# Kernel tuning notes

Measured on AMD Instinct MI355X. Metric: run time of the kernel, lower is better.

The kernel has to match this reference:

```python
import jax, jax.numpy as jnp
import numpy as np

HID = 1024
DEPTH = 2

def _rhn_layer(x, Win, bin_, Wh, bh, Wt, bt):
    # x: [B, T, in]; returns outputs [B, T, H]
    B = x.shape[0]
    h0 = jnp.zeros((B, HID), dtype=x.dtype)
    xt = jnp.swapaxes(x, 0, 1)  # [T, B, in]

    def step(h_prev, x_t):
        h = x_t @ Win + bin_
        for i in range(DEPTH):
            t_gate = jax.nn.sigmoid(h @ Wt[i] + bt[i])
            h_layer = jnp.tanh(h @ Wh[i] + bh[i])
            h = t_gate * h_layer + (1.0 - t_gate) * h
        h_new = h + h_prev
        return h_new, h_new

    _, outs = jax.lax.scan(step, h0, xt)  # [T, B, H]
    return jnp.swapaxes(outs, 0, 1)


def setup_inputs() -> dict:
    key = jax.random.key(0)
    ks = jax.random.split(key, 16)
    B, T, IN, H, OUT = 64, 256, 128, HID, 128
    s = lambda fan_in: 1.0 / np.sqrt(fan_in)
    d = {}
    d["x"] = jax.random.normal(ks[0], (B, T, IN), dtype=jnp.float32)
    # layer 0 (input_size=IN)
    d["l0_Win"] = jax.random.uniform(ks[1], (IN, H), minval=-s(IN), maxval=s(IN))
    d["l0_bin"] = jax.random.uniform(ks[2], (H,), minval=-s(IN), maxval=s(IN))
    d["l0_Wh"] = jax.random.uniform(ks[3], (DEPTH, H, H), minval=-s(H), maxval=s(H))
    d["l0_bh"] = jax.random.uniform(ks[4], (DEPTH, H), minval=-s(H), maxval=s(H))
    d["l0_Wt"] = jax.random.uniform(ks[5], (DEPTH, H, H), minval=-s(H), maxval=s(H))
    d["l0_bt"] = jax.random.uniform(ks[6], (DEPTH, H), minval=-s(H), maxval=s(H))
    # layer 1 (input_size=H)
    d["l1_Win"] = jax.random.uniform(ks[7], (H, H), minval=-s(H), maxval=s(H))
    d["l1_bin"] = jax.random.uniform(ks[8], (H,), minval=-s(H), maxval=s(H))
    d["l1_Wh"] = jax.random.uniform(ks[9], (DEPTH, H, H), minval=-s(H), maxval=s(H))
    d["l1_bh"] = jax.random.uniform(ks[10], (DEPTH, H), minval=-s(H), maxval=s(H))
    d["l1_Wt"] = jax.random.uniform(ks[11], (DEPTH, H, H), minval=-s(H), maxval=s(H))
    d["l1_bt"] = jax.random.uniform(ks[12], (DEPTH, H), minval=-s(H), maxval=s(H))
    # final fc
    d["fc_W"] = jax.random.uniform(ks[13], (H, OUT), minval=-s(H), maxval=s(H))
    d["fc_b"] = jax.random.uniform(ks[14], (OUT,), minval=-s(H), maxval=s(H))
    return d


def reference(x, l0_Win, l0_bin, l0_Wh, l0_bh, l0_Wt, l0_bt,
              l1_Win, l1_bin, l1_Wh, l1_bh, l1_Wt, l1_bt, fc_W, fc_b):
    out = _rhn_layer(x, l0_Win, l0_bin, l0_Wh, l0_bh, l0_Wt, l0_bt)
    out = _rhn_layer(out, l1_Win, l1_bin, l1_Wh, l1_bh, l1_Wt, l1_bt)
    # forecast_horizon = 1 -> last time step only
    out = out[:, -1:, :] @ fc_W + fc_b  # [B, 1, OUT]
    return out
```

## Files before the change

kernel.cpp:

```cpp
#include <hip/hip_runtime.h>

typedef unsigned short u16;
typedef unsigned int u32;
typedef __bf16 bf16x8 __attribute__((ext_vector_type(8)));
typedef float floatx4 __attribute__((ext_vector_type(4)));

#define HID 1024
#define BATCH 64
#define SEQ 256
#define INDIM 128
#define OUTDIM 128
#define MROWS (BATCH*SEQ)
#define CUMP 140

__device__ __forceinline__ float b2f(u16 u) {
    union { u32 u; float f; } v; v.u = ((u32)u) << 16; return v.f;
}
__device__ __forceinline__ u16 f2b(float f) {
    union { float f; u32 u; } v; v.f = f;
    u32 x = v.u;
    x += 0x7fffu + ((x >> 16) & 1u);
    return (u16)(x >> 16);
}
__device__ __forceinline__ float sigm(float x) { return 1.f / (1.f + __expf(-x)); }
__device__ __forceinline__ float tanh_f(float x) { return 2.f / (1.f + __expf(-2.f * x)) - 1.f; }

__device__ __forceinline__ void gld16(const u16* g, u16* l) {
    __builtin_amdgcn_global_load_lds(
        (const __attribute__((address_space(1))) void*)g,
        (__attribute__((address_space(3))) void*)l, 16, 0, 0);
}

__device__ __forceinline__ void bar_sync() {
    asm volatile("" ::: "memory");
    __builtin_amdgcn_s_barrier();
    asm volatile("" ::: "memory");
}
template <int N>
__device__ __forceinline__ void vm_bar() {
    asm volatile("s_waitcnt vmcnt(%0)" :: "n"(N) : "memory");
    __builtin_amdgcn_s_barrier();
    asm volatile("" ::: "memory");
}

__device__ __forceinline__ int is_fp32(const u16* probe, int tid) {
    const int lane = tid & 63;
    const int e = (probe[lane * 7] >> 7) & 0xff;
    return __ballot(e >= 127) != 0ULL;
}

struct CvtList { const void* s[8]; u16* d[8]; int n[8]; };

__global__ void convert8(CvtList C, const u16* __restrict__ probe) {
    const int fp32 = is_fp32(probe, threadIdx.x);
    const int z = blockIdx.y;
    const int n = C.n[z];
    const int stride = gridDim.x * 256;
    for (int i = blockIdx.x * 256 + threadIdx.x; i < n; i += stride) {
        u16 o;
        if (fp32) o = f2b(((const float*)C.s[z])[i]);
        else      o = ((const u16*)C.s[z])[i];
        C.d[z][i] = o;
    }
}

struct TListO {
    const void* s[10];
    u16*        d[10];
    int         R[10];
    int         Cc[10];
    long        off[10];
};

__global__ void transpose10(TListO L, const u16* __restrict__ probe) {
    const int tx = threadIdx.x, ty = threadIdx.y;
    const int fp32 = is_fp32(probe, ty * 32 + tx);
    const int z = blockIdx.z;
    const void* src = L.s[z];
    u16*        dst = L.d[z];
    const int R  = L.R[z];
    const int Cc = L.Cc[z];
    const long zo = L.off[z];
    const int tr = blockIdx.y * 32, tc = blockIdx.x * 32;
    if (tr >= R || tc >= Cc) return;
    __align__(16) __shared__ u16 t[32][33];
#pragma unroll
    for (int i = 0; i < 4; ++i) {
        const int r = ty + i * 8;
        const long e = zo + (long)(tr + r) * Cc + tc + tx;
        u16 v;
        if (fp32) v = f2b(((const float*)src)[e]);
        else      v = ((const u16*)src)[e];
        t[r][tx] = v;
    }
    __syncthreads();
#pragma unroll
    for (int i = 0; i < 4; ++i) {
        const int r = ty + i * 8;
        dst[(size_t)(tc + r) * R + tr + tx] = t[tx][r];
    }
}

__device__ __forceinline__ void tile_swizzle(int& m0, int& n0) {
    const int lin = blockIdx.y * gridDim.x + blockIdx.x;
    const int xcd = lin & 7;
    const int loc = lin >> 3;
    m0 = (xcd * 16 + (loc & 15)) * 128;
    n0 = (loc >> 4) * 128;
}

__device__ __forceinline__ void tile_swizzle8(int& m0, int& n0) {
    const int lin = blockIdx.x;
    const int xcd = lin & 7;
    const int loc = lin >> 3;
    m0 = (xcd * 8 + (loc & 7)) * 256;
    n0 = (loc >> 3) * 128;
}

__global__ __launch_bounds__(256, 2) void gemm128(
    const u16* __restrict__ A, const u16* __restrict__ BT,
    const u16* __restrict__ bias, u16* __restrict__ C,
    int M, int N, int K)
{
    __align__(16) __shared__ u16 As[128 * 64];
    __align__(16) __shared__ u16 Bs[128 * 64];

    const int tid  = threadIdx.x;
    const int lane = tid & 63;
    const int wid  = tid >> 6;
    const int wr   = wid >> 1;
    const int wc   = wid & 1;

    int m0, n0;
    tile_swizzle(m0, n0);

    floatx4 acc[4][4] = {};

    const int srow = lane >> 3;
    const int scol = 8 * ((lane & 7) ^ (lane >> 3));
    const int cb   = wid * 4;
    const u16* Ag[4]; const u16* Bg[4];
    u16 *Al[4], *Bl[4];
#pragma unroll
    for (int j = 0; j < 4; ++j) {
        const int c = cb + j;
        const int r = c * 8 + srow;
        Ag[j] = A  + (size_t)(m0 + r) * K + scol;
        Bg[j] = BT + (size_t)(n0 + r) * K + scol;
        Al[j] = As + c * 512;
        Bl[j] = Bs + c * 512;
    }

    const int quad = lane >> 4;
    const int l16  = lane & 15;
    const int swz  = l16 & 7;

    const int nk = K >> 6;
    for (int kt = 0; kt < nk; ++kt) {
        __syncthreads();
#pragma unroll
        for (int j = 0; j < 4; ++j) {
            gld16(Ag[j], Al[j]);  gld16(Bg[j], Bl[j]);
            Ag[j] += 64; Bg[j] += 64;
        }
        __syncthreads();

#pragma unroll
        for (int kk = 0; kk < 2; ++kk) {
            const int slot = ((kk * 4 + quad) ^ swz) * 8;
            bf16x8 af[4], bfr[4];
#pragma unroll
            for (int i = 0; i < 4; ++i) {
                af[i]  = *(const bf16x8*)(As + (wr * 64 + i * 16 + l16) * 64 + slot);
                bfr[i] = *(const bf16x8*)(Bs + (wc * 64 + i * 16 + l16) * 64 + slot);
            }
#pragma unroll
            for (int i = 0; i < 4; ++i)
#pragma unroll
                for (int j = 0; j < 4; ++j)
                    acc[i][j] = __builtin_amdgcn_mfma_f32_16x16x32_bf16(af[i], bfr[j], acc[i][j], 0, 0, 0);
        }
    }

#pragma unroll
    for (int i = 0; i < 4; ++i) {
        const int rowb = m0 + wr * 64 + i * 16 + quad * 4;
#pragma unroll
        for (int j = 0; j < 4; ++j) {
            const int col = n0 + wc * 64 + j * 16 + l16;
            const float bv = b2f(bias[col]);
#pragma unroll
            for (int r = 0; r < 4; ++r)
                C[(size_t)(rowb + r) * N + col] = f2b(acc[i][j][r] + bv);
        }
    }
}

__global__ __launch_bounds__(256, 2) void gemm_wp(
    const u16* __restrict__ At, const u16* __restrict__ Ah,
    const u16* __restrict__ BT, u16* __restrict__ Ct, u16* __restrict__ Ch)
{
    const u16* A = blockIdx.y ? Ah : At;
    u16*       C = blockIdx.y ? Ch : Ct;
    const int m0 = blockIdx.x * 128;
    const int K = HID, N = 128;

    __align__(16) __shared__ u16 As[128 * 64];
    __align__(16) __shared__ u16 Bs[128 * 64];

    const int tid  = threadIdx.x;
    const int lane = tid & 63;
    const int wid  = tid >> 6;
    const int wr   = wid >> 1;
    const int wc   = wid & 1;

    floatx4 acc[4][4] = {};

    const int srow = lane >> 3;
    const int scol = 8 * ((lane & 7) ^ (lane >> 3));
    const int cb   = wid * 4;
    const u16* Ag[4]; const u16* Bg[4];
    u16 *Al[4], *Bl[4];
#pragma unroll
    for (int j = 0; j < 4; ++j) {
        const int c = cb + j;
        const int r = c * 8 + srow;
        Ag[j] = A  + (size_t)(m0 + r) * K + scol;
        Bg[j] = BT + (size_t)r * K + scol;
        Al[j] = As + c * 512;
        Bl[j] = Bs + c * 512;
    }

    const int quad = lane >> 4;
    const int l16  = lane & 15;
    const int swz  = l16 & 7;

    for (int kt = 0; kt < (K >> 6); ++kt) {
        __syncthreads();
#pragma unroll
        for (int j = 0; j < 4; ++j) {
            gld16(Ag[j], Al[j]);  gld16(Bg[j], Bl[j]);
            Ag[j] += 64; Bg[j] += 64;
        }
        __syncthreads();

#pragma unroll
        for (int kk = 0; kk < 2; ++kk) {
            const int slot = ((kk * 4 + quad) ^ swz) * 8;
            bf16x8 af[4], bfr[4];
#pragma unroll
            for (int i = 0; i < 4; ++i) {
                af[i]  = *(const bf16x8*)(As + (wr * 64 + i * 16 + l16) * 64 + slot);
                bfr[i] = *(const bf16x8*)(Bs + (wc * 64 + i * 16 + l16) * 64 + slot);
            }
#pragma unroll
            for (int i = 0; i < 4; ++i)
#pragma unroll
                for (int j = 0; j < 4; ++j)
                    acc[i][j] = __builtin_amdgcn_mfma_f32_16x16x32_bf16(af[i], bfr[j], acc[i][j], 0, 0, 0);
        }
    }

#pragma unroll
    for (int i = 0; i < 4; ++i) {
        const int rowb = m0 + wr * 64 + i * 16 + quad * 4;
#pragma unroll
        for (int j = 0; j < 4; ++j) {
            const int col = wc * 64 + j * 16 + l16;
#pragma unroll
            for (int r = 0; r < 4; ++r)
                C[(size_t)(rowb + r) * N + col] = f2b(acc[i][j][r]);
        }
    }
}

__global__ void bias_fold(const u16* __restrict__ tWt, const u16* __restrict__ tWh,
                          const u16* __restrict__ binv, const u16* __restrict__ bt0,
                          const u16* __restrict__ bh0,
                          u16* __restrict__ obt, u16* __restrict__ obh)
{
    const u16* tW = blockIdx.y ? tWh : tWt;
    const u16* bo = blockIdx.y ? bh0 : bt0;
    u16*       ob = blockIdx.y ? obh : obt;
    const int j = blockIdx.x * 128 + threadIdx.x;
    const u16* row = tW + (size_t)j * HID;
    float acc = 0.f;
    for (int k = 0; k < HID; k += 8) {
        uint4 wv = *(const uint4*)(row + k);
        uint4 bv = *(const uint4*)(binv + k);
        const u16* w = (const u16*)&wv;
        const u16* b = (const u16*)&bv;
#pragma unroll
        for (int e = 0; e < 8; ++e) acc += b2f(b[e]) * b2f(w[e]);
    }
    ob[j] = f2b(acc + b2f(bo[j]));
}

__global__ __launch_bounds__(512, 2) void gemm_hw3(
    const u16* __restrict__ A,
    const u16* __restrict__ WtP,
    const u16* __restrict__ WhP,
    const u16* __restrict__ WiT,
    const u16* __restrict__ bpt, const u16* __restrict__ bph,
    const u16* __restrict__ bin,
    u16* __restrict__ Hout,
    int M, int N, int K)
{
    __align__(16) __shared__ u16 As [128 * 64];
    __align__(16) __shared__ u16 Bts[128 * 64];
    __align__(16) __shared__ u16 Bhs[128 * 64];
    __align__(16) __shared__ u16 Bis[128 * 64];

    const int tid  = threadIdx.x;
    const int lane = tid & 63;
    const int wid  = tid >> 6;
    const int wm   = wid >> 2;
    const int wn   = wid & 3;

    int m0, n0;
    tile_swizzle(m0, n0);

    floatx4 acct[4][2] = {};
    floatx4 acch[4][2] = {};
    floatx4 acci[4][2] = {};

    const int srow = lane >> 3;
    const int scol = 8 * ((lane & 7) ^ srow);
    const u16* Ag[2]; const u16* Tg[2]; const u16* Hg[2]; const u16* Ig[2];
    u16 *Al[2], *Tl[2], *Hl[2], *Il[2];
#pragma unroll
    for (int j = 0; j < 2; ++j) {
        const int c = wid * 2 + j;
        const int r = c * 8 + srow;
        Ag[j] = A   + (size_t)(m0 + r) * K + scol;
        Tg[j] = WtP + (size_t)(n0 + r) * K + scol;
        Hg[j] = WhP + (size_t)(n0 + r) * K + scol;
        Ig[j] = WiT + (size_t)(n0 + r) * K + scol;
        Al[j] = As  + c * 512;
        Tl[j] = Bts + c * 512;
        Hl[j] = Bhs + c * 512;
        Il[j] = Bis + c * 512;
    }

    const int quad = lane >> 4;
    const int l16  = lane & 15;
    const int swz  = l16 & 7;

    const int nk = K >> 6;
    for (int kt = 0; kt < nk; ++kt) {
        __syncthreads();
#pragma unroll
        for (int j = 0; j < 2; ++j) {
            gld16(Ag[j], Al[j]);  gld16(Tg[j], Tl[j]);
            gld16(Hg[j], Hl[j]);  gld16(Ig[j], Il[j]);
            Ag[j] += 64; Tg[j] += 64; Hg[j] += 64; Ig[j] += 64;
        }
        __syncthreads();

#pragma unroll
        for (int kk = 0; kk < 2; ++kk) {
            const int slot = ((kk * 4 + quad) ^ swz) * 8;
            bf16x8 af[4], btf[2], bhf[2], bif[2];
#pragma unroll
            for (int i = 0; i < 4; ++i)
                af[i] = *(const bf16x8*)(As + (wm * 64 + i * 16 + l16) * 64 + slot);
#pragma unroll
            for (int j = 0; j < 2; ++j) {
                btf[j] = *(const bf16x8*)(Bts + (wn * 32 + j * 16 + l16) * 64 + slot);
                bhf[j] = *(const bf16x8*)(Bhs + (wn * 32 + j * 16 + l16) * 64 + slot);
                bif[j] = *(const bf16x8*)(Bis + (wn * 32 + j * 16 + l16) * 64 + slot);
            }
#pragma unroll
            for (int i = 0; i < 4; ++i)
#pragma unroll
                for (int j = 0; j < 2; ++j) {
                    acct[i][j] = __builtin_amdgcn_mfma_f32_16x16x32_bf16(af[i], btf[j], acct[i][j], 0, 0, 0);
                    acch[i][j] = __builtin_amdgcn_mfma_f32_16x16x32_bf16(af[i], bhf[j], acch[i][j], 0, 0, 0);
                    acci[i][j] = __builtin_amdgcn_mfma_f32_16x16x32_bf16(af[i], bif[j], acci[i][j], 0, 0, 0);
                }
        }
    }

#pragma unroll
    for (int i = 0; i < 4; ++i) {
        const int rowb = m0 + wm * 64 + i * 16 + quad * 4;
#pragma unroll
        for (int j = 0; j < 2; ++j) {
            const int col = n0 + wn * 32 + j * 16 + l16;
            const float biv = b2f(bin[col]);
            const float btv = b2f(bpt[col]);
            const float bhv = b2f(bph[col]);
#pragma unroll
            for (int r = 0; r < 4; ++r) {
                const float h  = acci[i][j][r] + biv;
                const float tg = sigm(acct[i][j][r] + btv);
                const float hl = tanh_f(acch[i][j][r] + bhv);
                Hout[(size_t)(rowb + r) * N + col] = f2b(h + tg * (hl - h));
            }
        }
    }
}

__global__ __launch_bounds__(256, 2) void gemm_hw(
    const u16* __restrict__ A,
    const u16* __restrict__ WtT,
    const u16* __restrict__ WhT,
    const u16* __restrict__ bt, const u16* __restrict__ bh,
    u16* __restrict__ Hout,
    int M, int N, int K)
{
    __align__(16) __shared__ u16 As [128 * 64];
    __align__(16) __shared__ u16 Bts[128 * 64];
    __align__(16) __shared__ u16 Bhs[128 * 64];

    const int tid  = threadIdx.x;
    const int lane = tid & 63;
    const int wid  = tid >> 6;
    const int wr   = wid >> 1;
    const int wc   = wid & 1;

    int m0, n0;
    tile_swizzle(m0, n0);

    floatx4 acct[4][4] = {};
    floatx4 acch[4][4] = {};

    const int srow = lane >> 3;
    const int scol = 8 * ((lane & 7) ^ (lane >> 3));
    const int cb   = wid * 4;
    const u16* Ag[4]; const u16* Tg[4]; const u16* Hg[4];
    u16 *Al[4], *Tl[4], *Hl[4];
#pragma unroll
    for (int j = 0; j < 4; ++j) {
        const int c = cb + j;
        const int r = c * 8 + srow;
        Ag[j] = A   + (size_t)(m0 + r) * K + scol;
        Tg[j] = WtT + (size_t)(n0 + r) * K + scol;
        Hg[j] = WhT + (size_t)(n0 + r) * K + scol;
        Al[j] = As  + c * 512;
        Tl[j] = Bts + c * 512;
        Hl[j] = Bhs + c * 512;
    }

    const int quad = lane >> 4;
    const int l16  = lane & 15;
    const int swz  = l16 & 7;

    const int nk = K >> 6;
    for (int kt = 0; kt < nk; ++kt) {
        __syncthreads();
#pragma unroll
        for (int j = 0; j < 4; ++j) {
            gld16(Ag[j], Al[j]);  gld16(Tg[j], Tl[j]);  gld16(Hg[j], Hl[j]);
            Ag[j] += 64; Tg[j] += 64; Hg[j] += 64;
        }
        __syncthreads();

#pragma unroll
        for (int kk = 0; kk < 2; ++kk) {
            const int slot = ((kk * 4 + quad) ^ swz) * 8;
            bf16x8 af[4], btf[4], bhf[4];
#pragma unroll
            for (int i = 0; i < 4; ++i) {
                af[i]  = *(const bf16x8*)(As  + (wr * 64 + i * 16 + l16) * 64 + slot);
                btf[i] = *(const bf16x8*)(Bts + (wc * 64 + i * 16 + l16) * 64 + slot);
                bhf[i] = *(const bf16x8*)(Bhs + (wc * 64 + i * 16 + l16) * 64 + slot);
            }
#pragma unroll
            for (int i = 0; i < 4; ++i)
#pragma unroll
                for (int j = 0; j < 4; ++j) {
                    acct[i][j] = __builtin_amdgcn_mfma_f32_16x16x32_bf16(af[i], btf[j], acct[i][j], 0, 0, 0);
                    acch[i][j] = __builtin_amdgcn_mfma_f32_16x16x32_bf16(af[i], bhf[j], acch[i][j], 0, 0, 0);
                }
        }
    }

#pragma unroll
    for (int i = 0; i < 4; ++i) {
        const int rowb = m0 + wr * 64 + i * 16 + quad * 4;
#pragma unroll
        for (int j = 0; j < 4; ++j) {
            const int col = n0 + wc * 64 + j * 16 + l16;
            const float btv = b2f(bt[col]);
            const float bhv = b2f(bh[col]);
#pragma unroll
            for (int r = 0; r < 4; ++r) {
                const size_t idx = (size_t)(rowb + r) * N + col;
                const float hold = b2f(A[idx]);
                const float tg = sigm(acct[i][j][r] + btv);
                const float hl = tanh_f(acch[i][j][r] + bhv);
                Hout[idx] = f2b(hold + tg * (hl - hold));
            }
        }
    }
}

__global__ __launch_bounds__(256, 2) void gemm_hw_sum(
    const u16* __restrict__ A,
    const u16* __restrict__ WtT,
    const u16* __restrict__ WhT,
    const u16* __restrict__ bt, const u16* __restrict__ bh,
    float* __restrict__ hpart,
    int M, int N, int K)
{
    __align__(16) __shared__ u16 As [128 * 64];
    __align__(16) __shared__ u16 Bts[128 * 64];
    __align__(16) __shared__ u16 Bhs[128 * 64];

    const int tid  = threadIdx.x;
    const int lane = tid & 63;
    const int wid  = tid >> 6;
    const int wr   = wid >> 1;
    const int wc   = wid & 1;

    int m0, n0;
    tile_swizzle(m0, n0);

    floatx4 acct[4][4] = {};
    floatx4 acch[4][4] = {};

    const int srow = lane >> 3;
    const int scol = 8 * ((lane & 7) ^ (lane >> 3));
    const int cb   = wid * 4;
    const u16* Ag[4]; const u16* Tg[4]; const u16* Hg[4];
    u16 *Al[4], *Tl[4], *Hl[4];
#pragma unroll
    for (int j = 0; j < 4; ++j) {
        const int c = cb + j;
        const int r = c * 8 + srow;
        Ag[j] = A   + (size_t)(m0 + r) * K + scol;
        Tg[j] = WtT + (size_t)(n0 + r) * K + scol;
        Hg[j] = WhT + (size_t)(n0 + r) * K + scol;
        Al[j] = As  + c * 512;
        Tl[j] = Bts + c * 512;
        Hl[j] = Bhs + c * 512;
    }

    const int quad = lane >> 4;
    const int l16  = lane & 15;
    const int swz  = l16 & 7;

    const int nk = K >> 6;
    for (int kt = 0; kt < nk; ++kt) {
        __syncthreads();
#pragma unroll
        for (int j = 0; j < 4; ++j) {
            gld16(Ag[j], Al[j]);  gld16(Tg[j], Tl[j]);  gld16(Hg[j], Hl[j]);
            Ag[j] += 64; Tg[j] += 64; Hg[j] += 64;
        }
        __syncthreads();

#pragma unroll
        for (int kk = 0; kk < 2; ++kk) {
            const int slot = ((kk * 4 + quad) ^ swz) * 8;
            bf16x8 af[4], btf[4], bhf[4];
#pragma unroll
            for (int i = 0; i < 4; ++i) {
                af[i]  = *(const bf16x8*)(As  + (wr * 64 + i * 16 + l16) * 64 + slot);
                btf[i] = *(const bf16x8*)(Bts + (wc * 64 + i * 16 + l16) * 64 + slot);
                bhf[i] = *(const bf16x8*)(Bhs + (wc * 64 + i * 16 + l16) * 64 + slot);
            }
#pragma unroll
            for (int i = 0; i < 4; ++i)
#pragma unroll
                for (int j = 0; j < 4; ++j) {
                    acct[i][j] = __builtin_amdgcn_mfma_f32_16x16x32_bf16(af[i], btf[j], acct[i][j], 0, 0, 0);
                    acch[i][j] = __builtin_amdgcn_mfma_f32_16x16x32_bf16(af[i], bhf[j], acch[i][j], 0, 0, 0);
                }
        }
    }

    const int b    = m0 >> 8;
    const int slot = ((m0 >> 7) & 1) * 2 + wr;
#pragma unroll
    for (int j = 0; j < 4; ++j) {
        const int col = n0 + wc * 64 + j * 16 + l16;
        const float btv = b2f(bt[col]);
        const float bhv = b2f(bh[col]);
        float colsum = 0.f;
#pragma unroll
        for (int i = 0; i < 4; ++i) {
            const int rowb = m0 + wr * 64 + i * 16 + quad * 4;
#pragma unroll
            for (int r = 0; r < 4; ++r) {
                const size_t idx = (size_t)(rowb + r) * N + col;
                const float hold = b2f(A[idx]);
                const float tg = sigm(acct[i][j][r] + btv);
                const float hl = tanh_f(acch[i][j][r] + bhv);
                colsum += hold + tg * (hl - hold);
            }
        }
        colsum += __shfl_xor(colsum, 16, 64);
        colsum += __shfl_xor(colsum, 32, 64);
        if (quad == 0)
            hpart[((size_t)(slot * BATCH + b)) * HID + col] = colsum;
    }
}

__device__ __forceinline__ void hw8_mainloop(
    u16* lds,
    const u16* __restrict__ A, const u16* __restrict__ WtT, const u16* __restrict__ WhT,
    int m0, int n0, int K,
    floatx4 (&acct)[4][4], floatx4 (&acch)[4][4])
{
    const int tid  = threadIdx.x;
    const int lane = tid & 63;
    const int wid  = tid >> 6;
    const int wr   = wid >> 1;
    const int wc   = wid & 1;

    const int srow = lane >> 3;
    const int scol = 8 * ((lane & 7) ^ srow);

    const u16* Ag = A   + (size_t)(m0 + wid * 32 + srow) * K + scol;
    const u16* Tg = WtT + (size_t)(n0 + wid * 16 + srow) * K + scol;
    const u16* Hg = WhT + (size_t)(n0 + wid * 16 + srow) * K + scol;
    const size_t K8 = (size_t)K * 8;

    u16* dA = lds + wid * 2048;
    u16* dT = lds + 16384 + wid * 1024;
    u16* dH = lds + 24576 + wid * 1024;

    const int quad = lane >> 4;
    const int l16  = lane & 15;
    const int swz  = l16 & 7;
    const int s0 = (quad ^ swz) * 8;
    const int s1 = ((4 + quad) ^ swz) * 8;
    const int ra = wr * 64 + l16;
    const int rb = wc * 64 + l16;

    gld16(Tg,           dT);
    gld16(Tg +     K8,  dT + 512);
    gld16(Ag,           dA);
    gld16(Ag +     K8,  dA + 512);
    gld16(Ag + 2 * K8,  dA + 1024);
    gld16(Ag + 3 * K8,  dA + 1536);
    gld16(Hg,           dH);
    gld16(Hg +     K8,  dH + 512);
    Ag += 64; Tg += 64; Hg += 64;
    vm_bar<2>();

    const int nk = K >> 6;
    for (int kt = 0; kt < nk; ++kt) {
        const int  cur = kt & 1;
        const int  nb  = (cur ^ 1) * 32768;
        const bool pf  = (kt + 1 < nk);
        const u16* Sa = lds + cur * 32768;
        const u16* St = Sa + 16384;
        const u16* Sh = Sa + 24576;

        bf16x8 af0[4], af1[4], bq[4];

#pragma unroll
        for (int i = 0; i < 4; ++i) {
            af0[i] = *(const bf16x8*)(Sa + (ra + i * 16) * 64 + s0);
            bq[i]  = *(const bf16x8*)(St + (rb + i * 16) * 64 + s0);
        }
        if (pf) {
            gld16(Tg,      dT + nb);  gld16(Tg + K8, dT + nb + 512);
            gld16(Ag,      dA + nb);  gld16(Ag + K8, dA + nb + 512);
        }
        bar_sync();
        __builtin_amdgcn_s_setprio(1);
#pragma unroll
        for (int i = 0; i < 4; ++i)
#pragma unroll
            for (int j = 0; j < 4; ++j)
                acct[i][j] = __builtin_amdgcn_mfma_f32_16x16x32_bf16(af0[i], bq[j], acct[i][j], 0, 0, 0);
        __builtin_amdgcn_s_setprio(0);

#pragma unroll
        for (int i = 0; i < 4; ++i) {
            af1[i] = *(const bf16x8*)(Sa + (ra + i * 16) * 64 + s1);
            bq[i]  = *(const bf16x8*)(St + (rb + i * 16) * 64 + s1);
        }
        if (pf) {
            gld16(Ag + 2 * K8, dA + nb + 1024);
            gld16(Ag + 3 * K8, dA + nb + 1536);
            vm_bar<6>();
        } else {
            vm_bar<0>();
        }
        __builtin_amdgcn_s_setprio(1);
#pragma unroll
        for (int i = 0; i < 4; ++i)
#pragma unroll
            for (int j = 0; j < 4; ++j)
                acct[i][j] = __builtin_amdgcn_mfma_f32_16x16x32_bf16(af1[i], bq[j], acct[i][j], 0, 0, 0);
        __builtin_amdgcn_s_setprio(0);

#pragma unroll
        for (int i = 0; i < 4; ++i)
            bq[i] = *(const bf16x8*)(Sh + (rb + i * 16) * 64 + s0);
        bar_sync();
        __builtin_amdgcn_s_setprio(1);
#pragma unroll
        for (int i = 0; i < 4; ++i)
#pragma unroll
            for (int j = 0; j < 4; ++j)
                acch[i][j] = __builtin_amdgcn_mfma_f32_16x16x32_bf16(af0[i], bq[j], acch[i][j], 0, 0, 0);
        __builtin_amdgcn_s_setprio(0);

#pragma unroll
        for (int i = 0; i < 4; ++i)
            bq[i] = *(const bf16x8*)(Sh + (rb + i * 16) * 64 + s1);
        if (pf) {
            gld16(Hg,      dH + nb);
            gld16(Hg + K8, dH + nb + 512);
            vm_bar<2>();
        } else {
            bar_sync();
        }
        __builtin_amdgcn_s_setprio(1);
#pragma unroll
        for (int i = 0; i < 4; ++i)
#pragma unroll
            for (int j = 0; j < 4; ++j)
                acch[i][j] = __builtin_amdgcn_mfma_f32_16x16x32_bf16(af1[i], bq[j], acch[i][j], 0, 0, 0);
        __builtin_amdgcn_s_setprio(0);

        Ag += 64; Tg += 64; Hg += 64;
    }
}

__global__ __launch_bounds__(512, 2) void gemm_hw8_cum(
    const u16* __restrict__ A,
    const u16* __restrict__ WtT,
    const u16* __restrict__ WhT,
    const u16* __restrict__ bt, const u16* __restrict__ bh,
    u16* __restrict__ Y,
    int M, int N, int K)
{
    __align__(16) __shared__ u16 lds[65536];
    __shared__ float tot[512];

    int m0, n0;
    tile_swizzle8(m0, n0);

    floatx4 acct[4][4] = {};
    floatx4 acch[4][4] = {};
    hw8_mainloop(lds, A, WtT, WhT, m0, n0, K, acct, acch);

    const int tid  = threadIdx.x;
    const int lane = tid & 63;
    const int wid  = tid >> 6;
    const int wr   = wid >> 1;
    const int wc   = wid & 1;
    const int quad = lane >> 4;
    const int l16  = lane & 15;

    __syncthreads();

#pragma unroll
    for (int i = 0; i < 4; ++i) {
        const int rowl = wr * 64 + i * 16 + quad * 4;
#pragma unroll
        for (int j = 0; j < 4; ++j) {
            const int coll = wc * 64 + j * 16 + l16;
            const float btv = b2f(bt[n0 + coll]);
            const float bhv = b2f(bh[n0 + coll]);
#pragma unroll
            for (int r = 0; r < 4; ++r) {
                const size_t idx = (size_t)(m0 + rowl + r) * N + n0 + coll;
                const float hold = b2f(A[idx]);
                const float tg = sigm(acct[i][j][r] + btv);
                const float hl = tanh_f(acch[i][j][r] + bhv);
                lds[(rowl + r) * CUMP + coll] = f2b(hold + tg * (hl - hold));
            }
        }
    }
    __syncthreads();

    const int seg  = tid >> 7;
    const int colc = tid & 127;
    const int base = seg * 64 * CUMP + colc;
    {
        float local = 0.f;
#pragma unroll 8
        for (int t = 0; t < 64; ++t)
            local += b2f(lds[base + t * CUMP]);
        tot[seg * 128 + colc] = local;
    }
    __syncthreads();
    {
        float off = 0.f;
#pragma unroll
        for (int s = 0; s < 3; ++s)
            off += (s < seg) ? tot[s * 128 + colc] : 0.f;
        float acc = off;
#pragma unroll 8
        for (int t = 0; t < 64; ++t) {
            const int o = base + t * CUMP;
            acc += b2f(lds[o]);
            lds[o] = f2b(acc);
        }
    }
    __syncthreads();

#pragma unroll
    for (int it = 0; it < 16; ++it) {
        const int o   = it * 2048 + tid * 4;
        const int row = o >> 7;
        const int col = o & 127;
        *(uint2*)&Y[(size_t)(m0 + row) * N + n0 + col] =
            *(const uint2*)&lds[row * CUMP + col];
    }
}

__global__ void fc_final(const float* __restrict__ hp, const void* __restrict__ W,
                         const void* __restrict__ bias, void* __restrict__ out) {
    __shared__ float sh[HID];
    const int fp32 = is_fp32((const u16*)W, threadIdx.x);
    const int b = blockIdx.x, o = threadIdx.x;
    for (int k = o; k < HID; k += 128) {
        float v = 0.f;
#pragma unroll
        for (int s = 0; s < 4; ++s)
            v += hp[((size_t)(s * BATCH + b)) * HID + k];
        sh[k] = v;
    }
    __syncthreads();
    float acc;
    if (fp32) {
        acc = ((const float*)bias)[o];
        for (int k = 0; k < HID; ++k)
            acc += sh[k] * ((const float*)W)[(size_t)k * OUTDIM + o];
        ((float*)out)[b * OUTDIM + o] = acc;
    } else {
        acc = b2f(((const u16*)bias)[o]);
        for (int k = 0; k < HID; ++k)
            acc += sh[k] * b2f(((const u16*)W)[(size_t)k * OUTDIM + o]);
        ((u16*)out)[b * OUTDIM + o] = f2b(acc);
    }
}

extern "C" void kernel_launch(void* const* d_in, const int* in_sizes, int n_in,
                              void* d_out, int out_size, void* d_ws, size_t ws_size,
                              hipStream_t stream) {
    const void* x      = d_in[0];
    const void* l0_Win = d_in[1];
    const void* l0_bin = d_in[2];
    const void* l0_Wh  = d_in[3];
    const void* l0_bh  = d_in[4];
    const void* l0_Wt  = d_in[5];
    const void* l0_bt  = d_in[6];
    const void* l1_Win = d_in[7];
    const void* l1_bin = d_in[8];
    const void* l1_Wh  = d_in[9];
    const void* l1_bh  = d_in[10];
    const void* l1_Wt  = d_in[11];
    const void* l1_bt  = d_in[12];
    const void* fc_W   = d_in[13];
    const void* fc_b   = d_in[14];

    char* ws = (char*)d_ws;
    u16* Pa = (u16*)(ws);
    u16* Pb = (u16*)(ws + 33554432);
    u16* xc = Pb;
    u16* tW = (u16*)(ws + 67108864);
    u16* tWin0 = tW;
    u16* tWt00 = tWin0 + 131072;
    u16* tWt01 = tWt00 + 1048576;
    u16* tWh00 = tWt01 + 1048576;
    u16* tWh01 = tWh00 + 1048576;
    u16* tWin1 = tWh01 + 1048576;
    u16* tWt10 = tWin1 + 1048576;
    u16* tWt11 = tWt10 + 1048576;
    u16* tWh10 = tWt11 + 1048576;
    u16* tWh11 = tWh10 + 1048576;
    u16* smallb = tWh11 + 1048576;
    u16* binc0 = smallb;
    u16* bhc0  = binc0 + 1024;
    u16* btc0  = bhc0 + 2048;
    u16* binc1 = btc0 + 2048;
    u16* bhc1  = binc1 + 1024;
    u16* btc1  = bhc1 + 2048;
    u16* Win0c = btc1 + 2048;
    u16* Wpt   = Win0c + 131072;
    u16* Wph   = Wpt + 131072;
    u16* bpt   = Wph + 131072;
    u16* bph   = bpt + 1024;
    float* hpart = (float*)Pa;

    const u16* probe = (const u16*)l0_Wh;

    const long DD = (long)HID * HID;
    TListO L;
    L.s[0] = l0_Win; L.d[0] = tWin0; L.R[0] = INDIM; L.Cc[0] = HID; L.off[0] = 0;
    L.s[1] = l0_Wt;  L.d[1] = tWt00; L.R[1] = HID;   L.Cc[1] = HID; L.off[1] = 0;
    L.s[2] = l0_Wt;  L.d[2] = tWt01; L.R[2] = HID;   L.Cc[2] = HID; L.off[2] = DD;
    L.s[3] = l0_Wh;  L.d[3] = tWh00; L.R[3] = HID;   L.Cc[3] = HID; L.off[3] = 0;
    L.s[4] = l0_Wh;  L.d[4] = tWh01; L.R[4] = HID;   L.Cc[4] = HID; L.off[4] = DD;
    L.s[5] = l1_Win; L.d[5] = tWin1; L.R[5] = HID;   L.Cc[5] = HID; L.off[5] = 0;
    L.s[6] = l1_Wt;  L.d[6] = tWt10; L.R[6] = HID;   L.Cc[6] = HID; L.off[6] = 0;
    L.s[7] = l1_Wt;  L.d[7] = tWt11; L.R[7] = HID;   L.Cc[7] = HID; L.off[7] = DD;
    L.s[8] = l1_Wh;  L.d[8] = tWh10; L.R[8] = HID;   L.Cc[8] = HID; L.off[8] = 0;
    L.s[9] = l1_Wh;  L.d[9] = tWh11; L.R[9] = HID;   L.Cc[9] = HID; L.off[9] = DD;
    transpose10<<<dim3(32, 32, 10), dim3(32, 8), 0, stream>>>(L, probe);

    CvtList C8;
    C8.s[0] = x;      C8.d[0] = xc;    C8.n[0] = MROWS * INDIM;
    C8.s[1] = l0_bin; C8.d[1] = binc0; C8.n[1] = HID;
    C8.s[2] = l0_bh;  C8.d[2] = bhc0;  C8.n[2] = 2 * HID;
    C8.s[3] = l0_bt;  C8.d[3] = btc0;  C8.n[3] = 2 * HID;
    C8.s[4] = l1_bin; C8.d[4] = binc1; C8.n[4] = HID;
    C8.s[5] = l1_bh;  C8.d[5] = bhc1;  C8.n[5] = 2 * HID;
    C8.s[6] = l1_bt;  C8.d[6] = btc1;  C8.n[6] = 2 * HID;
    C8.s[7] = l0_Win; C8.d[7] = Win0c; C8.n[7] = INDIM * HID;
    convert8<<<dim3(512, 8), 256, 0, stream>>>(C8, probe);

    gemm_wp<<<dim3(8, 2), 256, 0, stream>>>(tWt00, tWh00, Win0c, Wpt, Wph);
    bias_fold<<<dim3(8, 2), 128, 0, stream>>>(tWt00, tWh00, binc0, btc0, bhc0, bpt, bph);

    gemm_hw3<<<dim3(8, 128), 512, 0, stream>>>(xc, Wpt, Wph, tWin0, bpt, bph, binc0,
                                               Pa, MROWS, HID, INDIM);
    gemm_hw8_cum<<<512, 512, 0, stream>>>(Pa, tWt01, tWh01, btc0 + HID, bhc0 + HID, Pb, MROWS, HID, HID);

    gemm128<<<dim3(8, 128), 256, 0, stream>>>(Pb, tWin1, binc1, Pa, MROWS, HID, HID);
    gemm_hw<<<dim3(8, 128), 256, 0, stream>>>(Pa, tWt10, tWh10, btc1, bhc1, Pb, MROWS, HID, HID);
    gemm_hw_sum<<<dim3(8, 128), 256, 0, stream>>>(Pb, tWt11, tWh11, btc1 + HID, bhc1 + HID,
                                                  hpart, MROWS, HID, HID);

    fc_final<<<64, 128, 0, stream>>>(hpart, fc_W, fc_b, d_out);
}
```

Baseline: 505.5 us.

## Merge prep kernels and replace pipelined hw8 mainloop with simple single-buffer loop

Folds the transpose and convert kernels into one launch and merges the bias-fold into the weight-product GEMM launch via an extra grid dimension, with the bias dot product split across two half-K thread groups. This removes several small kernel launches. It also replaces the double-buffered, interleaved hw8 mainloop with a single-buffered loop that loads, syncs and computes in turn. That shrinks LDS use but gives up overlap between global loads and MFMA work in the largest GEMM.

```diff
diff --git a/kernel.cpp b/kernel.cpp
--- a/kernel.cpp
+++ b/kernel.cpp
@@ -31,73 +31,57 @@
         (__attribute__((address_space(3))) void*)l, 16, 0, 0);
 }
 
-__device__ __forceinline__ void bar_sync() {
-    asm volatile("" ::: "memory");
-    __builtin_amdgcn_s_barrier();
-    asm volatile("" ::: "memory");
-}
-template <int N>
-__device__ __forceinline__ void vm_bar() {
-    asm volatile("s_waitcnt vmcnt(%0)" :: "n"(N) : "memory");
-    __builtin_amdgcn_s_barrier();
-    asm volatile("" ::: "memory");
-}
-
 __device__ __forceinline__ int is_fp32(const u16* probe, int tid) {
     const int lane = tid & 63;
     const int e = (probe[lane * 7] >> 7) & 0xff;
     return __ballot(e >= 127) != 0ULL;
 }
 
-struct CvtList { const void* s[8]; u16* d[8]; int n[8]; };
-
-__global__ void convert8(CvtList C, const u16* __restrict__ probe) {
-    const int fp32 = is_fp32(probe, threadIdx.x);
-    const int z = blockIdx.y;
-    const int n = C.n[z];
-    const int stride = gridDim.x * 256;
-    for (int i = blockIdx.x * 256 + threadIdx.x; i < n; i += stride) {
-        u16 o;
-        if (fp32) o = f2b(((const float*)C.s[z])[i]);
-        else      o = ((const u16*)C.s[z])[i];
-        C.d[z][i] = o;
-    }
-}
-
-struct TListO {
-    const void* s[10];
-    u16*        d[10];
-    int         R[10];
-    int         Cc[10];
-    long        off[10];
+struct PrepList {
+    const void* ts[10]; u16* td[10]; int tR[10]; int tC[10]; long toff[10];
+    const void* cs[8];  u16* cd[8];  int cn[8];
 };
 
-__global__ void transpose10(TListO L, const u16* __restrict__ probe) {
-    const int tx = threadIdx.x, ty = threadIdx.y;
-    const int fp32 = is_fp32(probe, ty * 32 + tx);
+__global__ void prep18(PrepList P, const u16* __restrict__ probe) {
+    const int tid  = threadIdx.x;
+    const int fp32 = is_fp32(probe, tid);
     const int z = blockIdx.z;
-    const void* src = L.s[z];
-    u16*        dst = L.d[z];
-    const int R  = L.R[z];
-    const int Cc = L.Cc[z];
-    const long zo = L.off[z];
-    const int tr = blockIdx.y * 32, tc = blockIdx.x * 32;
-    if (tr >= R || tc >= Cc) return;
-    __align__(16) __shared__ u16 t[32][33];
-#pragma unroll
-    for (int i = 0; i < 4; ++i) {
-        const int r = ty + i * 8;
-        const long e = zo + (long)(tr + r) * Cc + tc + tx;
-        u16 v;
-        if (fp32) v = f2b(((const float*)src)[e]);
-        else      v = ((const u16*)src)[e];
-        t[r][tx] = v;
-    }
-    __syncthreads();
-#pragma unroll
-    for (int i = 0; i < 4; ++i) {
-        const int r = ty + i * 8;
-        dst[(size_t)(tc + r) * R + tr + tx] = t[tx][r];
+    if (z < 10) {
+        const int tx = tid & 31, ty = tid >> 5;
+        const void* src = P.ts[z];
+        u16*        dst = P.td[z];
+        const int R  = P.tR[z];
+        const int Cc = P.tC[z];
+        const long zo = P.toff[z];
+        const int tr = blockIdx.y * 32, tc = blockIdx.x * 32;
+        if (tr >= R || tc >= Cc) return;
+        __align__(16) __shared__ u16 t[32][33];
+#pragma unroll
+        for (int i = 0; i < 4; ++i) {
+            const int r = ty + i * 8;
+            const long e = zo + (long)(tr + r) * Cc + tc + tx;
+            u16 v;
+            if (fp32) v = f2b(((const float*)src)[e]);
+            else      v = ((const u16*)src)[e];
+            t[r][tx] = v;
+        }
+        __syncthreads();
+#pragma unroll
+        for (int i = 0; i < 4; ++i) {
+            const int r = ty + i * 8;
+            dst[(size_t)(tc + r) * R + tr + tx] = t[tx][r];
+        }
+    } else {
+        const int c = z - 10;
+        const int n = P.cn[c];
+        const int lin = blockIdx.y * gridDim.x + blockIdx.x;
+        const int stride = gridDim.x * gridDim.y * 256;
+        for (int i = lin * 256 + tid; i < n; i += stride) {
+            u16 o;
+            if (fp32) o = f2b(((const float*)P.cs[c])[i]);
+            else      o = ((const u16*)P.cs[c])[i];
+            P.cd[c][i] = o;
+        }
     }
 }
 
@@ -196,10 +180,38 @@
     }
 }
 
-__global__ __launch_bounds__(256, 2) void gemm_wp(
+__global__ __launch_bounds__(256, 2) void gemm_wp_bias(
     const u16* __restrict__ At, const u16* __restrict__ Ah,
-    const u16* __restrict__ BT, u16* __restrict__ Ct, u16* __restrict__ Ch)
+    const u16* __restrict__ BT,
+    const u16* __restrict__ binv, const u16* __restrict__ bt0, const u16* __restrict__ bh0,
+    u16* __restrict__ Ct, u16* __restrict__ Ch,
+    u16* __restrict__ obt, u16* __restrict__ obh)
 {
+    const int tid = threadIdx.x;
+    if (blockIdx.z == 1) {
+        __shared__ float part[256];
+        const u16* tW = blockIdx.y ? Ah : At;
+        const u16* bo = blockIdx.y ? bh0 : bt0;
+        u16*       ob = blockIdx.y ? obh : obt;
+        const int j  = blockIdx.x * 128 + (tid & 127);
+        const int kh = tid >> 7;
+        const u16* row = tW + (size_t)j * HID + kh * 512;
+        float acc = 0.f;
+        for (int k = 0; k < 512; k += 8) {
+            uint4 wv = *(const uint4*)(row + k);
+            uint4 bv = *(const uint4*)(binv + kh * 512 + k);
+            const u16* w = (const u16*)&wv;
+            const u16* b = (const u16*)&bv;
+#pragma unroll
+            for (int e = 0; e < 8; ++e) acc += b2f(b[e]) * b2f(w[e]);
+        }
+        part[tid] = acc;
+        __syncthreads();
+        if (tid < 128)
+            ob[j] = f2b(part[tid] + part[tid + 128] + b2f(bo[j]));
+        return;
+    }
+
     const u16* A = blockIdx.y ? Ah : At;
     u16*       C = blockIdx.y ? Ch : Ct;
     const int m0 = blockIdx.x * 128;
@@ -208,7 +220,6 @@
     __align__(16) __shared__ u16 As[128 * 64];
     __align__(16) __shared__ u16 Bs[128 * 64];
 
-    const int tid  = threadIdx.x;
     const int lane = tid & 63;
     const int wid  = tid >> 6;
     const int wr   = wid >> 1;
@@ -272,28 +283,6 @@
                 C[(size_t)(rowb + r) * N + col] = f2b(acc[i][j][r]);
         }
     }
-}
-
-__global__ void bias_fold(const u16* __restrict__ tWt, const u16* __restrict__ tWh,
-                          const u16* __restrict__ binv, const u16* __restrict__ bt0,
-                          const u16* __restrict__ bh0,
-                          u16* __restrict__ obt, u16* __restrict__ obh)
-{
-    const u16* tW = blockIdx.y ? tWh : tWt;
-    const u16* bo = blockIdx.y ? bh0 : bt0;
-    u16*       ob = blockIdx.y ? obh : obt;
-    const int j = blockIdx.x * 128 + threadIdx.x;
-    const u16* row = tW + (size_t)j * HID;
-    float acc = 0.f;
-    for (int k = 0; k < HID; k += 8) {
-        uint4 wv = *(const uint4*)(row + k);
-        uint4 bv = *(const uint4*)(binv + k);
-        const u16* w = (const u16*)&wv;
-        const u16* b = (const u16*)&bv;
-#pragma unroll
-        for (int e = 0; e < 8; ++e) acc += b2f(b[e]) * b2f(w[e]);
-    }
-    ob[j] = f2b(acc + b2f(bo[j]));
 }
 
 __global__ __launch_bounds__(512, 2) void gemm_hw3(
@@ -598,132 +587,6 @@
     }
 }
 
-__device__ __forceinline__ void hw8_mainloop(
-    u16* lds,
-    const u16* __restrict__ A, const u16* __restrict__ WtT, const u16* __restrict__ WhT,
-    int m0, int n0, int K,
-    floatx4 (&acct)[4][4], floatx4 (&acch)[4][4])
-{
-    const int tid  = threadIdx.x;
-    const int lane = tid & 63;
-    const int wid  = tid >> 6;
-    const int wr   = wid >> 1;
-    const int wc   = wid & 1;
-
-    const int srow = lane >> 3;
-    const int scol = 8 * ((lane & 7) ^ srow);
-
-    const u16* Ag = A   + (size_t)(m0 + wid * 32 + srow) * K + scol;
-    const u16* Tg = WtT + (size_t)(n0 + wid * 16 + srow) * K + scol;
-    const u16* Hg = WhT + (size_t)(n0 + wid * 16 + srow) * K + scol;
-    const size_t K8 = (size_t)K * 8;
-
-    u16* dA = lds + wid * 2048;
-    u16* dT = lds + 16384 + wid * 1024;
-    u16* dH = lds + 24576 + wid * 1024;
-
-    const int quad = lane >> 4;
-    const int l16  = lane & 15;
-    const int swz  = l16 & 7;
-    const int s0 = (quad ^ swz) * 8;
-    const int s1 = ((4 + quad) ^ swz) * 8;
-    const int ra = wr * 64 + l16;
-    const int rb = wc * 64 + l16;
-
-    gld16(Tg,           dT);
-    gld16(Tg +     K8,  dT + 512);
-    gld16(Ag,           dA);
-    gld16(Ag +     K8,  dA + 512);
-    gld16(Ag + 2 * K8,  dA + 1024);
-    gld16(Ag + 3 * K8,  dA + 1536);
-    gld16(Hg,           dH);
-    gld16(Hg +     K8,  dH + 512);
-    Ag += 64; Tg += 64; Hg += 64;
-    vm_bar<2>();
-
-    const int nk = K >> 6;
-    for (int kt = 0; kt < nk; ++kt) {
-        const int  cur = kt & 1;
-        const int  nb  = (cur ^ 1) * 32768;
-        const bool pf  = (kt + 1 < nk);
-        const u16* Sa = lds + cur * 32768;
-        const u16* St = Sa + 16384;
-        const u16* Sh = Sa + 24576;
-
-        bf16x8 af0[4], af1[4], bq[4];
-
-#pragma unroll
-        for (int i = 0; i < 4; ++i) {
-            af0[i] = *(const bf16x8*)(Sa + (ra + i * 16) * 64 + s0);
-            bq[i]  = *(const bf16x8*)(St + (rb + i * 16) * 64 + s0);
-        }
-        if (pf) {
-            gld16(Tg,      dT + nb);  gld16(Tg + K8, dT + nb + 512);
-            gld16(Ag,      dA + nb);  gld16(Ag + K8, dA + nb + 512);
-        }
-        bar_sync();
-        __builtin_amdgcn_s_setprio(1);
-#pragma unroll
-        for (int i = 0; i < 4; ++i)
-#pragma unroll
-            for (int j = 0; j < 4; ++j)
-                acct[i][j] = __builtin_amdgcn_mfma_f32_16x16x32_bf16(af0[i], bq[j], acct[i][j], 0, 0, 0);
-        __builtin_amdgcn_s_setprio(0);
-
-#pragma unroll
-        for (int i = 0; i < 4; ++i) {
-            af1[i] = *(const bf16x8*)(Sa + (ra + i * 16) * 64 + s1);
-            bq[i]  = *(const bf16x8*)(St + (rb + i * 16) * 64 + s1);
-        }
-        if (pf) {
-            gld16(Ag + 2 * K8, dA + nb + 1024);
-            gld16(Ag + 3 * K8, dA + nb + 1536);
-            vm_bar<6>();
-        } else {
-            vm_bar<0>();
-        }
-        __builtin_amdgcn_s_setprio(1);
-#pragma unroll
-        for (int i = 0; i < 4; ++i)
-#pragma unroll
-            for (int j = 0; j < 4; ++j)
-                acct[i][j] = __builtin_amdgcn_mfma_f32_16x16x32_bf16(af1[i], bq[j], acct[i][j], 0, 0, 0);
-        __builtin_amdgcn_s_setprio(0);
-
-#pragma unroll
-        for (int i = 0; i < 4; ++i)
-            bq[i] = *(const bf16x8*)(Sh + (rb + i * 16) * 64 + s0);
-        bar_sync();
-        __builtin_amdgcn_s_setprio(1);
-#pragma unroll
-        for (int i = 0; i < 4; ++i)
-#pragma unroll
-            for (int j = 0; j < 4; ++j)
-                acch[i][j] = __builtin_amdgcn_mfma_f32_16x16x32_bf16(af0[i], bq[j], acch[i][j], 0, 0, 0);
-        __builtin_amdgcn_s_setprio(0);
-
-#pragma unroll
-        for (int i = 0; i < 4; ++i)
-            bq[i] = *(const bf16x8*)(Sh + (rb + i * 16) * 64 + s1);
-        if (pf) {
-            gld16(Hg,      dH + nb);
-            gld16(Hg + K8, dH + nb + 512);
-            vm_bar<2>();
-        } else {
-            bar_sync();
-        }
-        __builtin_amdgcn_s_setprio(1);
-#pragma unroll
-        for (int i = 0; i < 4; ++i)
-#pragma unroll
-            for (int j = 0; j < 4; ++j)
-                acch[i][j] = __builtin_amdgcn_mfma_f32_16x16x32_bf16(af1[i], bq[j], acch[i][j], 0, 0, 0);
-        __builtin_amdgcn_s_setprio(0);
-
-        Ag += 64; Tg += 64; Hg += 64;
-    }
-}
-
 __global__ __launch_bounds__(512, 2) void gemm_hw8_cum(
     const u16* __restrict__ A,
     const u16* __restrict__ WtT,
@@ -732,23 +595,75 @@
     u16* __restrict__ Y,
     int M, int N, int K)
 {
-    __align__(16) __shared__ u16 lds[65536];
+    __align__(16) __shared__ u16 lds[36864];
     __shared__ float tot[512];
-
-    int m0, n0;
-    tile_swizzle8(m0, n0);
-
-    floatx4 acct[4][4] = {};
-    floatx4 acch[4][4] = {};
-    hw8_mainloop(lds, A, WtT, WhT, m0, n0, K, acct, acch);
 
     const int tid  = threadIdx.x;
     const int lane = tid & 63;
     const int wid  = tid >> 6;
     const int wr   = wid >> 1;
     const int wc   = wid & 1;
+
+    int m0, n0;
+    tile_swizzle8(m0, n0);
+
+    floatx4 acct[4][4] = {};
+    floatx4 acch[4][4] = {};
+
+    const int srow = lane >> 3;
+    const int scol = 8 * ((lane & 7) ^ srow);
+    const u16* Ag[4]; const u16* Tg[2]; const u16* Hg[2];
+    u16 *Al[4], *Tl[2], *Hl[2];
+#pragma unroll
+    for (int j = 0; j < 4; ++j) {
+        const int c = wid * 4 + j;
+        Ag[j] = A + (size_t)(m0 + c * 8 + srow) * K + scol;
+        Al[j] = lds + c * 512;
+    }
+#pragma unroll
+    for (int j = 0; j < 2; ++j) {
+        const int c = wid * 2 + j;
+        Tg[j] = WtT + (size_t)(n0 + c * 8 + srow) * K + scol;
+        Hg[j] = WhT + (size_t)(n0 + c * 8 + srow) * K + scol;
+        Tl[j] = lds + 16384 + c * 512;
+        Hl[j] = lds + 24576 + c * 512;
+    }
+
     const int quad = lane >> 4;
     const int l16  = lane & 15;
+    const int swz  = l16 & 7;
+
+    const int nk = K >> 6;
+    for (int kt = 0; kt < nk; ++kt) {
+        __syncthreads();
+#pragma unroll
+        for (int j = 0; j < 4; ++j) { gld16(Ag[j], Al[j]); Ag[j] += 64; }
+#pragma unroll
+        for (int j = 0; j < 2; ++j) {
+            gld16(Tg[j], Tl[j]);  gld16(Hg[j], Hl[j]);
+            Tg[j] += 64; Hg[j] += 64;
+        }
+        __syncthreads();
+
+#pragma unroll
+        for (int kk = 0; kk < 2; ++kk) {
+            const int slot = ((kk * 4 + quad) ^ swz) * 8;
+            bf16x8 af[4], btf[4], bhf[4];
+#pragma unroll
+            for (int i = 0; i < 4; ++i) {
+                af[i]  = *(const bf16x8*)(lds +         (wr * 64 + i * 16 + l16) * 64 + slot);
+                btf[i] = *(const bf16x8*)(lds + 16384 + (wc * 64 + i * 16 + l16) * 64 + slot);
+                bhf[i] = *(const bf16x8*)(lds + 24576 + (wc * 64 + i * 16 + l16) * 64 + slot);
+            }
+#pragma unroll
+            for (int i = 0; i < 4; ++i)
+#pragma unroll
+                for (int j = 0; j < 4; ++j) {
+                    acct[i][j] = __builtin_amdgcn_mfma_f32_16x16x32_bf16(af[i], btf[j], acct[i][j], 0, 0, 0);
+                    acch[i][j] = __builtin_amdgcn_mfma_f32_16x16x32_bf16(af[i], bhf[j], acch[i][j], 0, 0, 0);
+                }
+        }
+    }
 
     __syncthreads();
 
@@ -886,32 +801,30 @@
     const u16* probe = (const u16*)l0_Wh;
 
     const long DD = (long)HID * HID;
-    TListO L;
-    L.s[0] = l0_Win; L.d[0] = tWin0; L.R[0] = INDIM; L.Cc[0] = HID; L.off[0] = 0;
-    L.s[1] = l0_Wt;  L.d[1] = tWt00; L.R[1] = HID;   L.Cc[1] = HID; L.off[1] = 0;
-    L.s[2] = l0_Wt;  L.d[2] = tWt01; L.R[2] = HID;   L.Cc[2] = HID; L.off[2] = DD;
-    L.s[3] = l0_Wh;  L.d[3] = tWh00; L.R[3] = HID;   L.Cc[3] = HID; L.off[3] = 0;
-    L.s[4] = l0_Wh;  L.d[4] = tWh01; L.R[4] = HID;   L.Cc[4] = HID; L.off[4] = DD;
-    L.s[5] = l1_Win; L.d[5] = tWin1; L.R[5] = HID;   L.Cc[5] = HID; L.off[5] = 0;
-    L.s[6] = l1_Wt;  L.d[6] = tWt10; L.R[6] = HID;   L.Cc[6] = HID; L.off[6] = 0;
-    L.s[7] = l1_Wt;  L.d[7] = tWt11; L.R[7] = HID;   L.Cc[7] = HID; L.off[7] = DD;
-    L.s[8] = l1_Wh;  L.d[8] = tWh10; L.R[8] = HID;   L.Cc[8] = HID; L.off[8] = 0;
-    L.s[9] = l1_Wh;  L.d[9] = tWh11; L.R[9] = HID;   L.Cc[9] = HID; L.off[9] = DD;
-    transpose10<<<dim3(32, 32, 10), dim3(32, 8), 0, stream>>>(L, probe);
-
-    CvtList C8;
-    C8.s[0] = x;      C8.d[0] = xc;    C8.n[0] = MROWS * INDIM;
-    C8.s[1] = l0_bin; C8.d[1] = binc0; C8.n[1] = HID;
-    C8.s[2] = l0_bh;  C8.d[2] = bhc0;  C8.n[2] = 2 * HID;
-    C8.s[3] = l0_bt;  C8.d[3] = btc0;  C8.n[3] = 2 * HID;
-    C8.s[4] = l1_bin; C8.d[4] = binc1; C8.n[4] = HID;
-    C8.s[5] = l1_bh;  C8.d[5] = bhc1;  C8.n[5] = 2 * HID;
-    C8.s[6] = l1_bt;  C8.d[6] = btc1;  C8.n[6] = 2 * HID;
-    C8.s[7] = l0_Win; C8.d[7] = Win0c; C8.n[7] = INDIM * HID;
-    convert8<<<dim3(512, 8), 256, 0, stream>>>(C8, probe);
-
-    gemm_wp<<<dim3(8, 2), 256, 0, stream>>>(tWt00, tWh00, Win0c, Wpt, Wph);
-    bias_fold<<<dim3(8, 2), 128, 0, stream>>>(tWt00, tWh00, binc0, btc0, bhc0, bpt, bph);
+    PrepList P;
+    P.ts[0] = l0_Win; P.td[0] = tWin0; P.tR[0] = INDIM; P.tC[0] = HID; P.toff[0] = 0;
+    P.ts[1] = l0_Wt;  P.td[1] = tWt00; P.tR[1] = HID;   P.tC[1] = HID; P.toff[1] = 0;
+    P.ts[2] = l0_Wt;  P.td[2] = tWt01; P.tR[2] = HID;   P.tC[2] = HID; P.toff[2] = DD;
+    P.ts[3] = l0_Wh;  P.td[3] = tWh00; P.tR[3] = HID;   P.tC[3] = HID; P.toff[3] = 0;
+    P.ts[4] = l0_Wh;  P.td[4] = tWh01; P.tR[4] = HID;   P.tC[4] = HID; P.toff[4] = DD;
+    P.ts[5] = l1_Win; P.td[5] = tWin1; P.tR[5] = HID;   P.tC[5] = HID; P.toff[5] = 0;
+    P.ts[6] = l1_Wt;  P.td[6] = tWt10; P.tR[6] = HID;   P.tC[6] = HID; P.toff[6] = 0;
+    P.ts[7] = l1_Wt;  P.td[7] = tWt11; P.tR[7] = HID;   P.tC[7] = HID; P.toff[7] = DD;
+    P.ts[8] = l1_Wh;  P.td[8] = tWh10; P.tR[8] = HID;   P.tC[8] = HID; P.toff[8] = 0;
+    P.ts[9] = l1_Wh;  P.td[9] = tWh11; P.tR[9] = HID;   P.tC[9] = HID; P.toff[9] = DD;
+    P.cs[0] = x;      P.cd[0] = xc;    P.cn[0] = MROWS * INDIM;
+    P.cs[1] = l0_bin; P.cd[1] = binc0; P.cn[1] = HID;
+    P.cs[2] = l0_bh;  P.cd[2] = bhc0;  P.cn[2] = 2 * HID;
+    P.cs[3] = l0_bt;  P.cd[3] = btc0;  P.cn[3] = 2 * HID;
+    P.cs[4] = l1_bin; P.cd[4] = binc1; P.cn[4] = HID;
+    P.cs[5] = l1_bh;  P.cd[5] = bhc1;  P.cn[5] = 2 * HID;
+    P.cs[6] = l1_bt;  P.cd[6] = btc1;  P.cn[6] = 2 * HID;
+    P.cs[7] = l0_Win; P.cd[7] = Win0c; P.cn[7] = INDIM * HID;
+    prep18<<<dim3(32, 32, 18), 256, 0, stream>>>(P, probe);
+
+    gemm_wp_bias<<<dim3(8, 2, 2), 256, 0, stream>>>(tWt00, tWh00, Win0c,
+                                                    binc0, btc0, bhc0,
+                                                    Wpt, Wph, bpt, bph);
 
     gemm_hw3<<<dim3(8, 128), 512, 0, stream>>>(xc, Wpt, Wph, tWin0, bpt, bph, binc0,
                                                Pa, MROWS, HID, INDIM);
```

Result: faster. 454.1 us (-10.2%).
